# Performance work log

Measured on AMD Instinct MI355X. Metric: run time of the kernel, lower is better.

## Reference

```python
import jax, jax.numpy as jnp
import numpy as np

N = 1024      # num_motifs == num_nodes (edge index i*N+j must fit in N*N table)
H = 128       # hidden_dim


def setup_inputs() -> dict:
    key = jax.random.key(0)
    k1, k2, k3, k4, k5, k6, k7 = jax.random.split(key, 7)
    s = 1.0 / np.sqrt(H)  # torch default init scale for Embedding-like/GRUCell params
    node_features = jax.random.normal(k1, (N, H), dtype=jnp.float32)
    adjacency_matrix = jax.random.randint(k2, (N, N), 0, 2, dtype=jnp.int32)
    edge_table = jax.random.normal(k3, (N * N, H), dtype=jnp.float32)  # nn.Embedding weight
    w_ih = jax.random.uniform(k4, (3 * H, H), minval=-s, maxval=s, dtype=jnp.float32)
    w_hh = jax.random.uniform(k5, (3 * H, H), minval=-s, maxval=s, dtype=jnp.float32)
    b_ih = jax.random.uniform(k6, (3 * H,), minval=-s, maxval=s, dtype=jnp.float32)
    b_hh = jax.random.uniform(k7, (3 * H,), minval=-s, maxval=s, dtype=jnp.float32)
    return {"node_features": node_features, "adjacency_matrix": adjacency_matrix,
            "edge_table": edge_table, "w_ih": w_ih, "w_hh": w_hh,
            "b_ih": b_ih, "b_hh": b_hh}


def reference(node_features, adjacency_matrix, edge_table, w_ih, w_hh, b_ih, b_hh):
    n, h = node_features.shape
    # edge embedding for edge (i, j) lives at row i*N + j -> view table as [N, N, H]
    T = edge_table.reshape(n, n, h)
    adj = adjacency_matrix.astype(node_features.dtype)
    # aggregated[i] = sum_{j : adj[i,j]=1} node_features[j] * edge_emb[i, j]
    agg = jnp.einsum('ij,jh,ijh->ih', adj, node_features, T)
    # GRUCell(input=agg, hidden=node_features), torch semantics
    gi = agg @ w_ih.T + b_ih              # [N, 3H]
    gh = node_features @ w_hh.T + b_hh    # [N, 3H]
    ir, iz, in_ = jnp.split(gi, 3, axis=-1)
    hr, hz, hn = jnp.split(gh, 3, axis=-1)
    r = jax.nn.sigmoid(ir + hr)
    z = jax.nn.sigmoid(iz + hz)
    nn_ = jnp.tanh(in_ + r * hn)
    return (1.0 - z) * nn_ + z * node_features
```

## Files before the change

kernel.cpp:

```cpp
#include <hip/hip_runtime.h>
#include <math.h>

#define N_NODES 1024
#define HDIM    128

__global__ __launch_bounds__(256) void motif_gru_kernel(
    const float* __restrict__ nf,
    const int*   __restrict__ adj,
    const float* __restrict__ T,
    const float* __restrict__ w_ih,
    const float* __restrict__ w_hh,
    const float* __restrict__ b_ih,
    const float* __restrict__ b_hh,
    float*       __restrict__ out)
{
    const int i   = blockIdx.x;
    const int tid = threadIdx.x;

    __shared__ int   s_list[N_NODES];
    __shared__ int   s_cnt;
    __shared__ float s_red[8][HDIM];
    __shared__ float s_agg[HDIM];
    __shared__ float s_nfi[HDIM];
    __shared__ float s_gi[3 * HDIM];
    __shared__ float s_gh[3 * HDIM];

    if (tid == 0) s_cnt = 0;
    __syncthreads();

    const int* adj_row = adj + (size_t)i * N_NODES;
    #pragma unroll
    for (int jj = 0; jj < N_NODES / 256; ++jj) {
        int j = tid + jj * 256;
        if (adj_row[j] != 0) {
            int pos = atomicAdd(&s_cnt, 1);
            s_list[pos] = j;
        }
    }
    if (tid < HDIM) s_nfi[tid] = nf[(size_t)i * HDIM + tid];
    __syncthreads();
    const int cnt = s_cnt;

    const int g    = tid >> 5;
    const int lane = tid & 31;

    const float4* Tv  = reinterpret_cast<const float4*>(T);
    const float4* nfv = reinterpret_cast<const float4*>(nf);
    const size_t rowbase = (size_t)i * N_NODES;

    float4 acc = make_float4(0.f, 0.f, 0.f, 0.f);

    int base = 0;
    for (; base + 16 <= cnt; base += 16) {
        int j0 = s_list[base + g];
        int j1 = s_list[base + 8 + g];
        float4 t0 = Tv[(rowbase + (size_t)j0) * 32 + lane];
        float4 n0 = nfv[(size_t)j0 * 32 + lane];
        float4 t1 = Tv[(rowbase + (size_t)j1) * 32 + lane];
        float4 n1 = nfv[(size_t)j1 * 32 + lane];
        acc.x += t0.x * n0.x; acc.y += t0.y * n0.y;
        acc.z += t0.z * n0.z; acc.w += t0.w * n0.w;
        acc.x += t1.x * n1.x; acc.y += t1.y * n1.y;
        acc.z += t1.z * n1.z; acc.w += t1.w * n1.w;
    }
    for (; base + 8 <= cnt; base += 8) {
        int j0 = s_list[base + g];
        float4 t0 = Tv[(rowbase + (size_t)j0) * 32 + lane];
        float4 n0 = nfv[(size_t)j0 * 32 + lane];
        acc.x += t0.x * n0.x; acc.y += t0.y * n0.y;
        acc.z += t0.z * n0.z; acc.w += t0.w * n0.w;
    }
    if (base + g < cnt) {
        int j0 = s_list[base + g];
        float4 t0 = Tv[(rowbase + (size_t)j0) * 32 + lane];
        float4 n0 = nfv[(size_t)j0 * 32 + lane];
        acc.x += t0.x * n0.x; acc.y += t0.y * n0.y;
        acc.z += t0.z * n0.z; acc.w += t0.w * n0.w;
    }

    reinterpret_cast<float4*>(&s_red[g][0])[lane] = acc;
    __syncthreads();

    if (tid < HDIM) {
        float s = 0.f;
        #pragma unroll
        for (int gg = 0; gg < 8; ++gg) s += s_red[gg][tid];
        s_agg[tid] = s;
    }
    __syncthreads();

    const float4* aggv = reinterpret_cast<const float4*>(s_agg);
    const float4* nfiv = reinterpret_cast<const float4*>(s_nfi);
    for (int c = tid; c < 3 * HDIM; c += 256) {
        const float4* wi = reinterpret_cast<const float4*>(w_ih + (size_t)c * HDIM);
        const float4* wh = reinterpret_cast<const float4*>(w_hh + (size_t)c * HDIM);
        float gs = 0.f, hs = 0.f;
        #pragma unroll 8
        for (int k = 0; k < HDIM / 4; ++k) {
            float4 w4 = wi[k]; float4 a4 = aggv[k];
            gs += w4.x * a4.x + w4.y * a4.y + w4.z * a4.z + w4.w * a4.w;
            float4 v4 = wh[k]; float4 n4 = nfiv[k];
            hs += v4.x * n4.x + v4.y * n4.y + v4.z * n4.z + v4.w * n4.w;
        }
        s_gi[c] = gs + b_ih[c];
        s_gh[c] = hs + b_hh[c];
    }
    __syncthreads();

    if (tid < HDIM) {
        float r  = 1.f / (1.f + expf(-(s_gi[tid] + s_gh[tid])));
        float z  = 1.f / (1.f + expf(-(s_gi[HDIM + tid] + s_gh[HDIM + tid])));
        float nn = tanhf(s_gi[2 * HDIM + tid] + r * s_gh[2 * HDIM + tid]);
        out[(size_t)i * HDIM + tid] = (1.f - z) * nn + z * s_nfi[tid];
    }
}

extern "C" void kernel_launch(void* const* d_in, const int* in_sizes, int n_in,
                              void* d_out, int out_size, void* d_ws, size_t ws_size,
                              hipStream_t stream) {
    const float* nf   = (const float*)d_in[0];
    const int*   adj  = (const int*)d_in[1];
    const float* T    = (const float*)d_in[2];
    const float* w_ih = (const float*)d_in[3];
    const float* w_hh = (const float*)d_in[4];
    const float* b_ih = (const float*)d_in[5];
    const float* b_hh = (const float*)d_in[6];
    float* out = (float*)d_out;

    motif_gru_kernel<<<dim3(N_NODES), dim3(256), 0, stream>>>(
        nf, adj, T, w_ih, w_hh, b_ih, b_hh, out);
}
```

Baseline: 677.2 us.

## Use ballot-based ordered neighbor list, 512 threads, prefetched nontemporal gather loop

Replaces atomic-based neighbor list compaction with wave ballot/popcount prefix sums, giving a sorted list without atomics. Doubles block size to 512 threads and restructures the gather loop into a one-ahead software pipeline using nontemporal loads for the streaming edge table. Splits the GRU gate GEMVs so all threads each compute one dot product. Risk: the pipeline keeps fewer loads in flight per thread than the prior 2-way unroll.

```diff
diff --git a/kernel.cpp b/kernel.cpp
--- a/kernel.cpp
+++ b/kernel.cpp
@@ -3,8 +3,13 @@
 
 #define N_NODES 1024
 #define HDIM    128
+#define NT      512
+#define NG      (NT / 32)
+#define NW      (NT / 64)
 
-__global__ __launch_bounds__(256) void motif_gru_kernel(
+typedef float floatx4 __attribute__((ext_vector_type(4)));
+
+__global__ __launch_bounds__(NT, 8) void motif_gru_kernel(
     const float* __restrict__ nf,
     const int*   __restrict__ adj,
     const float* __restrict__ T,
@@ -18,99 +23,118 @@
     const int tid = threadIdx.x;
 
     __shared__ int   s_list[N_NODES];
+    __shared__ int   s_wcnt[NW];
+    __shared__ int   s_woff[NW];
     __shared__ int   s_cnt;
-    __shared__ float s_red[8][HDIM];
+    __shared__ float s_red[NG][HDIM];
     __shared__ float s_agg[HDIM];
     __shared__ float s_nfi[HDIM];
     __shared__ float s_gi[3 * HDIM];
     __shared__ float s_gh[3 * HDIM];
 
-    if (tid == 0) s_cnt = 0;
-    __syncthreads();
+    const int w      = tid >> 6;
+    const int lane64 = tid & 63;
 
     const int* adj_row = adj + (size_t)i * N_NODES;
-    #pragma unroll
-    for (int jj = 0; jj < N_NODES / 256; ++jj) {
-        int j = tid + jj * 256;
-        if (adj_row[j] != 0) {
-            int pos = atomicAdd(&s_cnt, 1);
-            s_list[pos] = j;
-        }
+    const int  jbase   = w * (N_NODES / NW);
+    const int  a0 = adj_row[jbase + lane64];
+    const int  a1 = adj_row[jbase + 64 + lane64];
+    const unsigned long long m0 = __ballot(a0 != 0);
+    const unsigned long long m1 = __ballot(a1 != 0);
+    const int c0 = __popcll(m0);
+    if (lane64 == 0) s_wcnt[w] = c0 + __popcll(m1);
+    if (tid < HDIM) s_nfi[tid] = nf[(size_t)i * HDIM + tid];
+    __syncthreads();
+    if (tid == 0) {
+        int s = 0;
+        #pragma unroll
+        for (int ww = 0; ww < NW; ++ww) { s_woff[ww] = s; s += s_wcnt[ww]; }
+        s_cnt = s;
     }
-    if (tid < HDIM) s_nfi[tid] = nf[(size_t)i * HDIM + tid];
+    __syncthreads();
+    {
+        const unsigned long long below = (1ull << lane64) - 1ull;
+        const int off = s_woff[w];
+        if (a0) s_list[off + __popcll(m0 & below)]      = jbase + lane64;
+        if (a1) s_list[off + c0 + __popcll(m1 & below)] = jbase + 64 + lane64;
+    }
     __syncthreads();
     const int cnt = s_cnt;
 
     const int g    = tid >> 5;
     const int lane = tid & 31;
 
-    const float4* Tv  = reinterpret_cast<const float4*>(T);
-    const float4* nfv = reinterpret_cast<const float4*>(nf);
-    const size_t rowbase = (size_t)i * N_NODES;
+    const floatx4* Tv  = reinterpret_cast<const floatx4*>(T) + (size_t)i * N_NODES * 32;
+    const floatx4* nfv = reinterpret_cast<const floatx4*>(nf);
 
-    float4 acc = make_float4(0.f, 0.f, 0.f, 0.f);
+    floatx4 acc = (floatx4)(0.f);
 
-    int base = 0;
-    for (; base + 16 <= cnt; base += 16) {
-        int j0 = s_list[base + g];
-        int j1 = s_list[base + 8 + g];
-        float4 t0 = Tv[(rowbase + (size_t)j0) * 32 + lane];
-        float4 n0 = nfv[(size_t)j0 * 32 + lane];
-        float4 t1 = Tv[(rowbase + (size_t)j1) * 32 + lane];
-        float4 n1 = nfv[(size_t)j1 * 32 + lane];
-        acc.x += t0.x * n0.x; acc.y += t0.y * n0.y;
-        acc.z += t0.z * n0.z; acc.w += t0.w * n0.w;
-        acc.x += t1.x * n1.x; acc.y += t1.y * n1.y;
-        acc.z += t1.z * n1.z; acc.w += t1.w * n1.w;
+    int  rNext = g;
+    bool vB    = (rNext < cnt);
+    floatx4 tB = (floatx4)(0.f);
+    floatx4 nB = (floatx4)(0.f);
+    if (vB) {
+        const int j = s_list[rNext];
+        tB = __builtin_nontemporal_load(&Tv[(size_t)j * 32 + lane]);
+        nB = nfv[(size_t)j * 32 + lane];
     }
-    for (; base + 8 <= cnt; base += 8) {
-        int j0 = s_list[base + g];
-        float4 t0 = Tv[(rowbase + (size_t)j0) * 32 + lane];
-        float4 n0 = nfv[(size_t)j0 * 32 + lane];
-        acc.x += t0.x * n0.x; acc.y += t0.y * n0.y;
-        acc.z += t0.z * n0.z; acc.w += t0.w * n0.w;
-    }
-    if (base + g < cnt) {
-        int j0 = s_list[base + g];
-        float4 t0 = Tv[(rowbase + (size_t)j0) * 32 + lane];
-        float4 n0 = nfv[(size_t)j0 * 32 + lane];
-        acc.x += t0.x * n0.x; acc.y += t0.y * n0.y;
-        acc.z += t0.z * n0.z; acc.w += t0.w * n0.w;
+    rNext += NG;
+    bool vNext = (rNext < cnt);
+    int  jNext = vNext ? s_list[rNext] : 0;
+
+    while (vB) {
+        floatx4 tC = (floatx4)(0.f);
+        floatx4 nC = (floatx4)(0.f);
+        const bool vC = vNext;
+        if (vC) {
+            tC = __builtin_nontemporal_load(&Tv[(size_t)jNext * 32 + lane]);
+            nC = nfv[(size_t)jNext * 32 + lane];
+        }
+        rNext += NG;
+        vNext = (rNext < cnt);
+        jNext = vNext ? s_list[rNext] : 0;
+
+        acc += tB * nB;
+
+        tB = tC; nB = nC; vB = vC;
     }
 
-    reinterpret_cast<float4*>(&s_red[g][0])[lane] = acc;
+    *reinterpret_cast<floatx4*>(&s_red[g][lane * 4]) = acc;
     __syncthreads();
 
     if (tid < HDIM) {
         float s = 0.f;
         #pragma unroll
-        for (int gg = 0; gg < 8; ++gg) s += s_red[gg][tid];
+        for (int gg = 0; gg < NG; ++gg) s += s_red[gg][tid];
         s_agg[tid] = s;
     }
     __syncthreads();
 
-    const float4* aggv = reinterpret_cast<const float4*>(s_agg);
-    const float4* nfiv = reinterpret_cast<const float4*>(s_nfi);
-    for (int c = tid; c < 3 * HDIM; c += 256) {
-        const float4* wi = reinterpret_cast<const float4*>(w_ih + (size_t)c * HDIM);
-        const float4* wh = reinterpret_cast<const float4*>(w_hh + (size_t)c * HDIM);
-        float gs = 0.f, hs = 0.f;
-        #pragma unroll 8
+    const floatx4* aggv = reinterpret_cast<const floatx4*>(s_agg);
+    const floatx4* nfiv = reinterpret_cast<const floatx4*>(s_nfi);
+    for (int cc = tid; cc < 6 * HDIM; cc += NT) {
+        const bool isin = cc < 3 * HDIM;
+        const int  c    = isin ? cc : cc - 3 * HDIM;
+        const floatx4* wp = reinterpret_cast<const floatx4*>(
+            (isin ? w_ih : w_hh) + (size_t)c * HDIM);
+        const floatx4* xv = isin ? aggv : nfiv;
+        float s = 0.f;
+        #pragma unroll 4
         for (int k = 0; k < HDIM / 4; ++k) {
-            float4 w4 = wi[k]; float4 a4 = aggv[k];
-            gs += w4.x * a4.x + w4.y * a4.y + w4.z * a4.z + w4.w * a4.w;
-            float4 v4 = wh[k]; float4 n4 = nfiv[k];
-            hs += v4.x * n4.x + v4.y * n4.y + v4.z * n4.z + v4.w * n4.w;
+            floatx4 w4 = wp[k];
+            floatx4 x4 = xv[k];
+            floatx4 p  = w4 * x4;
+            s += p.x + p.y + p.z + p.w;
         }
-        s_gi[c] = gs + b_ih[c];
-        s_gh[c] = hs + b_hh[c];
+        if (isin) s_gi[c] = s + b_ih[c];
+        else      s_gh[c] = s + b_hh[c];
     }
     __syncthreads();
 
     if (tid < HDIM) {
-        float r  = 1.f / (1.f + expf(-(s_gi[tid] + s_gh[tid])));
-        float z  = 1.f / (1.f + expf(-(s_gi[HDIM + tid] + s_gh[HDIM + tid])));
-        float nn = tanhf(s_gi[2 * HDIM + tid] + r * s_gh[2 * HDIM + tid]);
+        const float r  = 1.f / (1.f + expf(-(s_gi[tid] + s_gh[tid])));
+        const float z  = 1.f / (1.f + expf(-(s_gi[HDIM + tid] + s_gh[HDIM + tid])));
+        const float nn = tanhf(s_gi[2 * HDIM + tid] + r * s_gh[2 * HDIM + tid]);
         out[(size_t)i * HDIM + tid] = (1.f - z) * nn + z * s_nfi[tid];
     }
 }
@@ -127,6 +151,6 @@
     const float* b_hh = (const float*)d_in[6];
     float* out = (float*)d_out;
 
-    motif_gru_kernel<<<dim3(N_NODES), dim3(256), 0, stream>>>(
+    motif_gru_kernel<<<dim3(N_NODES), dim3(NT), 0, stream>>>(
         nf, adj, T, w_ih, w_hh, b_ih, b_hh, out);
 }
```

Result: no change. 667.9 us (-1.4%).
